# Performance work log

Hardware: AMD Instinct MI355X
Metric: run time of the kernel (lower is better)

The kernel has to match this reference:

```python
import jax, jax.numpy as jnp
import numpy as np

N = 100000
E = 1600000
D_IN = 64
D_OUT = 64
EPS = 1e-5  # PyG LayerNorm eps


def setup_inputs() -> dict:
    key = jax.random.key(0)
    k1, k2, k3, k4 = jax.random.split(key, 4)
    x = jax.random.normal(k1, (N, D_IN), dtype=jnp.float32)
    edge_index = jax.random.randint(k2, (2, E), 0, N, dtype=jnp.int32)
    edge_weight = jax.random.uniform(k3, (E,), dtype=jnp.float32)
    # GCNConv params: Linear(D_IN, D_OUT, bias=True) -> weight [D_OUT, D_IN]
    W = jax.random.normal(k4, (D_OUT, D_IN), dtype=jnp.float32) * (1.0 / np.sqrt(D_IN))
    b = jnp.zeros((D_OUT,), dtype=jnp.float32)
    # LayerNorm affine params (per-feature)
    gamma = jnp.ones((D_OUT,), dtype=jnp.float32)
    beta = jnp.zeros((D_OUT,), dtype=jnp.float32)
    return {"x": x, "edge_index": edge_index, "edge_weight": edge_weight,
            "W": W, "b": b, "gamma": gamma, "beta": beta}


def reference(x, edge_index, edge_weight, W, b, gamma, beta):
    # --- GCNConv with symmetric normalization and self-loops ---
    n = x.shape[0]
    loop = jnp.arange(n, dtype=edge_index.dtype)
    src = jnp.concatenate([edge_index[0], loop])          # [E+N]
    dst = jnp.concatenate([edge_index[1], loop])          # [E+N]
    w = jnp.concatenate([edge_weight, jnp.ones((n,), x.dtype)])
    deg = jax.ops.segment_sum(w, dst, num_segments=n)     # weighted in-degree
    dis = jnp.where(deg > 0, jax.lax.rsqrt(deg), 0.0)     # deg^{-1/2}
    norm = dis[src] * w * dis[dst]                        # [E+N]
    xw = x @ W.T                                          # [N, D_OUT]
    msgs = xw[src] * norm[:, None]                        # gather + scale
    out = jax.ops.segment_sum(msgs, dst, num_segments=n) + b
    # --- PyG LayerNorm mode='graph' (single graph): mean/var over all entries ---
    mu = out.mean()
    var = jnp.mean((out - mu) ** 2)
    out = (out - mu) * jax.lax.rsqrt(var + EPS) * gamma + beta
    # --- activation (ReLU), norm_first=False -> act(norm(x)) ---
    return jax.nn.relu(out)
```

## Files before the change

kernel.cpp:

```cpp
#include <hip/hip_runtime.h>
#include <hip/hip_fp16.h>
#include <math.h>

#define D 64
#define LN_EPS 1e-5f
#define SCAN_CH 1024
#define WFIX 262144.0f
#define CNT_SH 25
#define WSUM_MASK ((1u << CNT_SH) - 1)
#define WQ_BITS 15
#define WQ_SCALE 32768.0f
#define NB 1024
#define BSH 7
#define GP 256


__global__ __launch_bounds__(256) void k_hist1(const int* __restrict__ ei, int E,
                                               int* __restrict__ hist) {
    __shared__ int h[NB];
    for (int i = threadIdx.x; i < NB; i += 256) h[i] = 0;
    __syncthreads();
    int chunk = (E + GP - 1) / GP;
    int s0 = blockIdx.x * chunk;
    int s1 = min(E, s0 + chunk);
    for (int e = s0 + threadIdx.x; e < s1; e += 256)
        atomicAdd(&h[((unsigned int)ei[E + e]) >> BSH], 1);
    __syncthreads();
    for (int i = threadIdx.x; i < NB; i += 256)
        hist[i * GP + blockIdx.x] = h[i];
}

__global__ __launch_bounds__(256) void k_scanb(int* __restrict__ hist,
                                               int* __restrict__ total) {
    int lane = threadIdx.x & 63, wv = threadIdx.x >> 6;
    int bucket = blockIdx.x * 4 + wv;
    int4 c = *(int4*)&hist[bucket * GP + lane * 4];
    int lsum = c.x + c.y + c.z + c.w;
    int sum = lsum;
#pragma unroll
    for (int off2 = 1; off2 < 64; off2 <<= 1) {
        int t = __shfl_up(sum, off2);
        if (lane >= off2) sum += t;
    }
    int base = sum - lsum;
    int4 o;
    o.x = base; o.y = base + c.x; o.z = o.y + c.y; o.w = o.z + c.z;
    *(int4*)&hist[bucket * GP + lane * 4] = o;
    if (lane == 63) total[bucket] = sum;
}

__global__ __launch_bounds__(SCAN_CH) void k_scan_base(int* __restrict__ psum, int nblk) {
    __shared__ int s[SCAN_CH];
    int tid = threadIdx.x;
    s[tid] = (tid < nblk) ? psum[tid] : 0;
    __syncthreads();
    int own = s[tid];
    for (int off = 1; off < SCAN_CH; off <<= 1) {
        int t = (tid >= off) ? s[tid - off] : 0;
        __syncthreads();
        s[tid] += t;
        __syncthreads();
    }
    if (tid < nblk) psum[tid] = s[tid] - own;
}

__global__ __launch_bounds__(256) void k_part(const int* __restrict__ ei,
                                              const float* __restrict__ w,
                                              const int* __restrict__ hist,
                                              const int* __restrict__ total,
                                              unsigned long long* __restrict__ part,
                                              int E) {
    __shared__ int cur[NB];
    for (int i = threadIdx.x; i < NB; i += 256)
        cur[i] = total[i] + hist[i * GP + blockIdx.x];
    __syncthreads();
    int chunk = (E + GP - 1) / GP;
    int s0 = blockIdx.x * chunk;
    int s1 = min(E, s0 + chunk);
    for (int e = s0 + threadIdx.x; e < s1; e += 256) {
        unsigned int dst = (unsigned int)ei[E + e];
        unsigned int src = (unsigned int)ei[e];
        float wf = w[e];
        int pos = atomicAdd(&cur[dst >> BSH], 1);
        unsigned int wq = __float2uint_rn(wf * WQ_SCALE);
        if (wq > 32767u) wq = 32767u;
        unsigned int wfix = __float2uint_rn(wf * WFIX);
        unsigned int lo = (src << WQ_BITS) | wq;
        unsigned int hi = (dst & ((1u << BSH) - 1)) | (wfix << BSH);
        part[pos] = ((unsigned long long)hi << 32) | lo;
    }
}

__global__ __launch_bounds__(256) void k_emit(const unsigned long long* __restrict__ part,
                                              const int* __restrict__ total,
                                              unsigned int* __restrict__ packed,
                                              int* __restrict__ nstart,
                                              unsigned int* __restrict__ csr,
                                              int N, int E) {
    __shared__ unsigned int cw[1 << BSH];
    __shared__ int cursor[1 << BSH];
    __shared__ int wtot[2];
    int b = blockIdx.x;
    int beg = total[b];
    int end = (b == NB - 1) ? E : total[b + 1];
    int tid = threadIdx.x;
    if (tid < (1 << BSH)) cw[tid] = 0;
    __syncthreads();
    for (int i = beg + tid; i < end; i += 256) {
        unsigned int hi = (unsigned int)(part[i] >> 32);
        atomicAdd(&cw[hi & 127u], (1u << CNT_SH) | (hi >> BSH));
    }
    __syncthreads();
    int lane = tid & 63, wv = tid >> 6;
    if (tid < 128) {
        unsigned int p = cw[tid];
        int cnt = (int)(p >> CNT_SH);
        int sum = cnt;
#pragma unroll
        for (int off2 = 1; off2 < 64; off2 <<= 1) {
            int t = __shfl_up(sum, off2);
            if (lane >= off2) sum += t;
        }
        if (lane == 63) wtot[wv] = sum;
        cursor[tid] = sum - cnt;
        int node = (b << BSH) + tid;
        if (node < N) packed[node] = p;
    }
    __syncthreads();
    if (tid < 128) {
        int st = cursor[tid] + beg + ((wv == 1) ? wtot[0] : 0);
        cursor[tid] = st;
        int node = (b << BSH) + tid;
        if (node < N) nstart[node] = st;
    }
    __syncthreads();
    for (int i = beg + tid; i < end; i += 256) {
        unsigned long long r = part[i];
        unsigned int hi = (unsigned int)(r >> 32);
        int pos = atomicAdd(&cursor[hi & 127u], 1);
        csr[pos] = (unsigned int)r;
    }
}

__global__ __launch_bounds__(256, 4) void k_gemm(const float* __restrict__ x,
                                                 const float* __restrict__ W,
                                                 const unsigned int* __restrict__ packed,
                                                 __half* __restrict__ y, int N) {
    __shared__ float Ws[D * 68];
    __shared__ float xs[64 * 68];
    int tid = threadIdx.x;
    int rowBase = blockIdx.x * 64;
#pragma unroll
    for (int i = 0; i < 16; ++i) {
        int idx = i * 256 + tid;
        int a = idx >> 6, kk = idx & 63;
        Ws[a * 68 + kk] = W[idx];
        int row = rowBase + a;
        xs[a * 68 + kk] = (row < N) ? x[idx + rowBase * D] : 0.0f;
    }
    __syncthreads();
    int l = tid & 63, wv = tid >> 6;
    int g = l >> 4;
    int c1 = l & 15;
    int r0 = wv * 16 + g * 4;
    float acc[4][4];
#pragma unroll
    for (int a = 0; a < 4; ++a)
#pragma unroll
        for (int bj = 0; bj < 4; ++bj) acc[a][bj] = 0.0f;
#pragma unroll 2
    for (int kc = 0; kc < 16; ++kc) {
        int k0 = kc * 4;
        float4 xr[4], wr[4];
#pragma unroll
        for (int jr = 0; jr < 4; ++jr)
            xr[jr] = *(const float4*)&xs[(r0 + jr) * 68 + k0];
#pragma unroll
        for (int jc = 0; jc < 4; ++jc)
            wr[jc] = *(const float4*)&Ws[(c1 + 16 * jc) * 68 + k0];
#pragma unroll
        for (int jr = 0; jr < 4; ++jr)
#pragma unroll
            for (int jc = 0; jc < 4; ++jc)
                acc[jr][jc] += xr[jr].x * wr[jc].x + xr[jr].y * wr[jc].y +
                               xr[jr].z * wr[jc].z + xr[jr].w * wr[jc].w;
    }
#pragma unroll
    for (int jr = 0; jr < 4; ++jr) {
        int row = rowBase + r0 + jr;
        if (row < N) {
            float dr = rsqrtf(1.0f +
                (float)(packed[row] & WSUM_MASK) * (1.0f / WFIX));
#pragma unroll
            for (int jc = 0; jc < 4; ++jc)
                y[row * D + c1 + 16 * jc] = __float2half_rn(acc[jr][jc] * dr);
        }
    }
}

__global__ __launch_bounds__(256) void k_gather(const unsigned int* __restrict__ packed,
                                                const int* __restrict__ nstart,
                                                const unsigned int* __restrict__ csr,
                                                const __half* __restrict__ y,
                                                const float* __restrict__ b,
                                                float* __restrict__ out,
                                                float* __restrict__ partial, int N) {
    int wid = (blockIdx.x * 256 + threadIdx.x) >> 6;
    int lane = threadIdx.x & 63;
    float s = 0.0f, ss = 0.0f;
    if (wid < N) {
        int n = wid;
        unsigned int p = packed[n];
        int m = (int)(p >> CNT_SH);
        int start = nstart[n];
        float dis_n = rsqrtf(1.0f + (float)(p & WSUM_MASK) * (1.0f / WFIX));
        float acc = __half2float(y[(size_t)n * D + lane]);
        const float wsc = 1.0f / WQ_SCALE;
        for (int base0 = start; base0 < start + m; base0 += 64) {
            int mm = start + m - base0; if (mm > 64) mm = 64;
            unsigned int pe = (lane < mm) ? csr[base0 + lane] : 0u;
            int j = 0;
            for (; j + 3 < mm; j += 4) {
                unsigned int p0 = __shfl(pe, j);
                unsigned int p1 = __shfl(pe, j + 1);
                unsigned int p2 = __shfl(pe, j + 2);
                unsigned int p3 = __shfl(pe, j + 3);
                float a0 = __half2float(y[(size_t)(p0 >> WQ_BITS) * D + lane]);
                float a1 = __half2float(y[(size_t)(p1 >> WQ_BITS) * D + lane]);
                float a2 = __half2float(y[(size_t)(p2 >> WQ_BITS) * D + lane]);
                float a3 = __half2float(y[(size_t)(p3 >> WQ_BITS) * D + lane]);
                acc += (float)(p0 & 32767u) * wsc * a0;
                acc += (float)(p1 & 32767u) * wsc * a1;
                acc += (float)(p2 & 32767u) * wsc * a2;
                acc += (float)(p3 & 32767u) * wsc * a3;
            }
            for (; j < mm; ++j) {
                unsigned int p0 = __shfl(pe, j);
                acc += (float)(p0 & 32767u) * wsc *
                       __half2float(y[(size_t)(p0 >> WQ_BITS) * D + lane]);
            }
        }
        float o = dis_n * acc + b[lane];
        out[(size_t)n * D + lane] = o;
        s = o;
        ss = o * o;
    }
#pragma unroll
    for (int off = 32; off; off >>= 1) {
        s += __shfl_down(s, off);
        ss += __shfl_down(ss, off);
    }
    __shared__ float ls[4], lss[4];
    int wv = threadIdx.x >> 6;
    if (lane == 0) { ls[wv] = s; lss[wv] = ss; }
    __syncthreads();
    if (threadIdx.x == 0) {
        partial[2 * blockIdx.x]     = ls[0] + ls[1] + ls[2] + ls[3];
        partial[2 * blockIdx.x + 1] = lss[0] + lss[1] + lss[2] + lss[3];
    }
}

__global__ __launch_bounds__(SCAN_CH) void k_redux(const float* __restrict__ partial,
                                                   int nb, double* __restrict__ scal) {
    double s = 0.0, ss = 0.0;
    for (int i = threadIdx.x; i < nb; i += SCAN_CH) {
        s += (double)partial[2 * i];
        ss += (double)partial[2 * i + 1];
    }
#pragma unroll
    for (int off = 32; off; off >>= 1) {
        s += __shfl_down(s, off);
        ss += __shfl_down(ss, off);
    }
    __shared__ double ls[SCAN_CH / 64], lss[SCAN_CH / 64];
    int lane = threadIdx.x & 63, wv = threadIdx.x >> 6;
    if (lane == 0) { ls[wv] = s; lss[wv] = ss; }
    __syncthreads();
    if (threadIdx.x == 0) {
        double S = 0.0, SS = 0.0;
        for (int k = 0; k < SCAN_CH / 64; ++k) { S += ls[k]; SS += lss[k]; }
        scal[0] = S;
        scal[1] = SS;
    }
}

__global__ __launch_bounds__(256) void k_ln(float* __restrict__ out,
                                            const float* __restrict__ gamma,
                                            const float* __restrict__ beta,
                                            const double* __restrict__ scal, int N) {
    int nchunks = N * (D / 4);
    int i = blockIdx.x * blockDim.x + threadIdx.x;
    if (i >= nchunks) return;
    double M = (double)N * (double)D;
    double mu = scal[0] / M;
    double var = scal[1] / M - mu * mu;
    float muf = (float)mu;
    float isd = (float)(1.0 / sqrt(var + (double)LN_EPS));
    int c4 = (i & 15) * 4;
    float4 v = ((float4*)out)[i];
    v.x = fmaxf((v.x - muf) * isd * gamma[c4 + 0] + beta[c4 + 0], 0.0f);
    v.y = fmaxf((v.y - muf) * isd * gamma[c4 + 1] + beta[c4 + 1], 0.0f);
    v.z = fmaxf((v.z - muf) * isd * gamma[c4 + 2] + beta[c4 + 2], 0.0f);
    v.w = fmaxf((v.w - muf) * isd * gamma[c4 + 3] + beta[c4 + 3], 0.0f);
    ((float4*)out)[i] = v;
}

__global__ __launch_bounds__(256) void k_build(const int* __restrict__ ei,
                                               const float* __restrict__ w,
                                               unsigned int* __restrict__ packed,
                                               int E) {
    int e = blockIdx.x * blockDim.x + threadIdx.x;
    if (e < E) {
        unsigned int v = (1u << CNT_SH) | __float2uint_rn(w[e] * WFIX);
        atomicAdd(&packed[ei[E + e]], v);
    }
}

__global__ __launch_bounds__(256) void k_scatter(const int* __restrict__ ei,
                                                 const float* __restrict__ w,
                                                 const __half* __restrict__ y,
                                                 float* __restrict__ out, int E) {
    int t = blockIdx.x * blockDim.x + threadIdx.x;
    int e = t >> 6;
    int lane = t & 63;
    if (e >= E) return;
    float v = w[e] * __half2float(y[(size_t)ei[e] * D + lane]);
    unsafeAtomicAdd(&out[(size_t)ei[E + e] * D + lane], v);
}

__global__ __launch_bounds__(256) void k_seed(const __half* __restrict__ y,
                                              float* __restrict__ out, int total) {
    int i = blockIdx.x * blockDim.x + threadIdx.x;
    if (i < total) out[i] = __half2float(y[i]);
}

__global__ __launch_bounds__(256) void k_finalize(float* __restrict__ out,
                                                  const unsigned int* __restrict__ packed,
                                                  const float* __restrict__ b,
                                                  double* __restrict__ scal, int N) {
    int nchunks = N * (D / 4);
    float s = 0.0f, ss = 0.0f;
    float4* o4 = (float4*)out;
    for (int i = blockIdx.x * blockDim.x + threadIdx.x; i < nchunks;
         i += gridDim.x * blockDim.x) {
        int row = i >> 4;
        int c4 = (i & 15) * 4;
        float4 v = o4[i];
        float dr = rsqrtf(1.0f + (float)(packed[row] & WSUM_MASK) * (1.0f / WFIX));
        v.x = dr * v.x + b[c4 + 0];
        v.y = dr * v.y + b[c4 + 1];
        v.z = dr * v.z + b[c4 + 2];
        v.w = dr * v.w + b[c4 + 3];
        o4[i] = v;
        s += v.x + v.y + v.z + v.w;
        ss += v.x * v.x + v.y * v.y + v.z * v.z + v.w * v.w;
    }
#pragma unroll
    for (int off = 32; off; off >>= 1) {
        s += __shfl_down(s, off);
        ss += __shfl_down(ss, off);
    }
    __shared__ float ls[4], lss[4];
    int lane = threadIdx.x & 63, wv = threadIdx.x >> 6;
    if (lane == 0) { ls[wv] = s; lss[wv] = ss; }
    __syncthreads();
    if (threadIdx.x == 0) {
        atomicAdd(&scal[0], (double)(ls[0] + ls[1] + ls[2] + ls[3]));
        atomicAdd(&scal[1], (double)(lss[0] + lss[1] + lss[2] + lss[3]));
    }
}

extern "C" void kernel_launch(void* const* d_in, const int* in_sizes, int n_in,
                              void* d_out, int out_size, void* d_ws, size_t ws_size,
                              hipStream_t stream) {
    const float* x     = (const float*)d_in[0];
    const int*   ei    = (const int*)d_in[1];
    const float* ew    = (const float*)d_in[2];
    const float* W     = (const float*)d_in[3];
    const float* b     = (const float*)d_in[4];
    const float* gamma = (const float*)d_in[5];
    const float* beta  = (const float*)d_in[6];
    float* out = (float*)d_out;

    int N = in_sizes[0] / D;
    int E = in_sizes[2];
    int gb = (N + 3) / 4;

    char* ws = (char*)d_ws;
    size_t off = 0;
    unsigned int* packed = (unsigned int*)(ws + off); off += (size_t)N * 4;
    int* nstart  = (int*)(ws + off);    off += (size_t)N * 4;
    int* hist    = (int*)(ws + off);    off += (size_t)NB * GP * 4;
    int* total   = (int*)(ws + off);    off += (size_t)NB * 4;
    double* scal = (double*)(ws + off); off += 16;
    float* partial = (float*)(ws + off); off += (size_t)gb * 8;
    off = (off + 255) & ~(size_t)255;
    size_t partBytes = (size_t)E * 8;
    size_t yBytes = (size_t)N * D * 2;
    unsigned long long* part = (unsigned long long*)(ws + off);
    __half* y = (__half*)(ws + off);
    off += (partBytes > yBytes) ? partBytes : yBytes;
    off = (off + 255) & ~(size_t)255;
    unsigned int* csr = (unsigned int*)(ws + off); off += (size_t)E * 4;

    int nbu = (N + (1 << BSH) - 1) >> BSH;
    bool csr_path = (ws_size >= off) && (N <= (1 << 17)) && (nbu <= NB) &&
                    ((size_t)E <= (size_t)N * 24);

    if (csr_path) {
        k_hist1<<<GP, 256, 0, stream>>>(ei, E, hist);
        k_scanb<<<NB / 4, 256, 0, stream>>>(hist, total);
        k_scan_base<<<1, SCAN_CH, 0, stream>>>(total, NB);
        k_part<<<GP, 256, 0, stream>>>(ei, ew, hist, total, part, E);
        k_emit<<<nbu, 256, 0, stream>>>(part, total, packed, nstart, csr, N, E);
        k_gemm<<<(N + 63) / 64, 256, 0, stream>>>(x, W, packed, y, N);
        k_gather<<<gb, 256, 0, stream>>>(packed, nstart, csr, y, b, out, partial, N);
        k_redux<<<1, SCAN_CH, 0, stream>>>(partial, gb, scal);
        k_ln<<<(N * (D / 4) + 255) / 256, 256, 0, stream>>>(out, gamma, beta, scal, N);
    } else {
        hipMemsetAsync(packed, 0, (size_t)N * 4, stream);
        hipMemsetAsync(scal, 0, 16, stream);
        k_build<<<(E + 255) / 256, 256, 0, stream>>>(ei, ew, packed, E);
        k_gemm<<<(N + 63) / 64, 256, 0, stream>>>(x, W, packed, y, N);
        k_seed<<<(N * D + 255) / 256, 256, 0, stream>>>(y, out, N * D);
        k_scatter<<<(E + 3) / 4, 256, 0, stream>>>(ei, ew, y, out, E);
        k_finalize<<<2048, 256, 0, stream>>>(out, packed, b, scal, N);
        k_ln<<<(N * (D / 4) + 255) / 256, 256, 0, stream>>>(out, gamma, beta, scal, N);
    }
}
```

Before: 241.6 us.

## Fuse scan and reduction kernels; grid-stride gather with scalar CSR loads

The single-block base scan is folded into the partition kernel: each block recomputes the 1024-entry bucket prefix itself and block 0 writes it out for the emit stage. The separate stats reduction kernel is removed, and every LayerNorm block now re-reduces the 2048 gather partials in double before normalising. The gather becomes a grid-stride loop over a fixed 2048-block grid, reading CSR entries as wave-uniform scalar loads instead of a lane load plus shuffles. Two launches are removed, at the cost of redundant per-block prefix and reduction work.

```diff
diff --git a/kernel.cpp b/kernel.cpp
--- a/kernel.cpp
+++ b/kernel.cpp
@@ -13,6 +13,7 @@
 #define NB 1024
 #define BSH 7
 #define GP 256
+#define GB2 2048
 
 
 __global__ __launch_bounds__(256) void k_hist1(const int* __restrict__ ei, int E,
@@ -49,39 +50,52 @@
     if (lane == 63) total[bucket] = sum;
 }
 
-__global__ __launch_bounds__(SCAN_CH) void k_scan_base(int* __restrict__ psum, int nblk) {
-    __shared__ int s[SCAN_CH];
+__global__ __launch_bounds__(256) void k_part2(const int* __restrict__ ei,
+                                               const float* __restrict__ w,
+                                               const int* __restrict__ hist,
+                                               const int* __restrict__ total,
+                                               int* __restrict__ total2,
+                                               unsigned long long* __restrict__ part,
+                                               int E) {
+    __shared__ int shB[NB];
+    __shared__ int shA[NB];
+    __shared__ int wt4[4];
     int tid = threadIdx.x;
-    s[tid] = (tid < nblk) ? psum[tid] : 0;
-    __syncthreads();
-    int own = s[tid];
-    for (int off = 1; off < SCAN_CH; off <<= 1) {
-        int t = (tid >= off) ? s[tid - off] : 0;
+    int lane = tid & 63, wv = tid >> 6;
+    {
+        int4 c4v = *(const int4*)&total[tid * 4];
+        int lsum = c4v.x + c4v.y + c4v.z + c4v.w;
+        int sum = lsum;
+#pragma unroll
+        for (int o2 = 1; o2 < 64; o2 <<= 1) {
+            int t = __shfl_up(sum, o2);
+            if (lane >= o2) sum += t;
+        }
+        if (lane == 63) wt4[wv] = sum;
         __syncthreads();
-        s[tid] += t;
-        __syncthreads();
-    }
-    if (tid < nblk) psum[tid] = s[tid] - own;
-}
-
-__global__ __launch_bounds__(256) void k_part(const int* __restrict__ ei,
-                                              const float* __restrict__ w,
-                                              const int* __restrict__ hist,
-                                              const int* __restrict__ total,
-                                              unsigned long long* __restrict__ part,
-                                              int E) {
-    __shared__ int cur[NB];
-    for (int i = threadIdx.x; i < NB; i += 256)
-        cur[i] = total[i] + hist[i * GP + blockIdx.x];
+        int woff = 0;
+#pragma unroll
+        for (int k = 0; k < 4; ++k) if (k < wv) woff += wt4[k];
+        int base = woff + sum - lsum;
+        shB[tid * 4 + 0] = base;
+        shB[tid * 4 + 1] = base + c4v.x;
+        shB[tid * 4 + 2] = base + c4v.x + c4v.y;
+        shB[tid * 4 + 3] = base + c4v.x + c4v.y + c4v.z;
+    }
+    __syncthreads();
+    if (blockIdx.x == 0)
+        *(int4*)&total2[tid * 4] = *(const int4*)&shB[tid * 4];
+    for (int i = tid; i < NB; i += 256)
+        shA[i] = shB[i] + hist[i * GP + blockIdx.x];
     __syncthreads();
     int chunk = (E + GP - 1) / GP;
     int s0 = blockIdx.x * chunk;
     int s1 = min(E, s0 + chunk);
-    for (int e = s0 + threadIdx.x; e < s1; e += 256) {
+    for (int e = s0 + tid; e < s1; e += 256) {
         unsigned int dst = (unsigned int)ei[E + e];
         unsigned int src = (unsigned int)ei[e];
         float wf = w[e];
-        int pos = atomicAdd(&cur[dst >> BSH], 1);
+        int pos = atomicAdd(&shA[dst >> BSH], 1);
         unsigned int wq = __float2uint_rn(wf * WQ_SCALE);
         if (wq > 32767u) wq = 32767u;
         unsigned int wfix = __float2uint_rn(wf * WFIX);
@@ -92,7 +106,7 @@
 }
 
 __global__ __launch_bounds__(256) void k_emit(const unsigned long long* __restrict__ part,
-                                              const int* __restrict__ total,
+                                              const int* __restrict__ total2,
                                               unsigned int* __restrict__ packed,
                                               int* __restrict__ nstart,
                                               unsigned int* __restrict__ csr,
@@ -101,8 +115,8 @@
     __shared__ int cursor[1 << BSH];
     __shared__ int wtot[2];
     int b = blockIdx.x;
-    int beg = total[b];
-    int end = (b == NB - 1) ? E : total[b + 1];
+    int beg = total2[b];
+    int end = (b == NB - 1) ? E : total2[b + 1];
     int tid = threadIdx.x;
     if (tid < (1 << BSH)) cw[tid] = 0;
     __syncthreads();
@@ -117,9 +131,9 @@
         int cnt = (int)(p >> CNT_SH);
         int sum = cnt;
 #pragma unroll
-        for (int off2 = 1; off2 < 64; off2 <<= 1) {
-            int t = __shfl_up(sum, off2);
-            if (lane >= off2) sum += t;
+        for (int o2 = 1; o2 < 64; o2 <<= 1) {
+            int t = __shfl_up(sum, o2);
+            if (lane >= o2) sum += t;
         }
         if (lane == 63) wtot[wv] = sum;
         cursor[tid] = sum - cnt;
@@ -198,52 +212,50 @@
     }
 }
 
-__global__ __launch_bounds__(256) void k_gather(const unsigned int* __restrict__ packed,
-                                                const int* __restrict__ nstart,
-                                                const unsigned int* __restrict__ csr,
-                                                const __half* __restrict__ y,
-                                                const float* __restrict__ b,
-                                                float* __restrict__ out,
-                                                float* __restrict__ partial, int N) {
-    int wid = (blockIdx.x * 256 + threadIdx.x) >> 6;
-    int lane = threadIdx.x & 63;
+__global__ __launch_bounds__(256) void k_gather2(const unsigned int* __restrict__ packed,
+                                                 const int* __restrict__ nstart,
+                                                 const unsigned int* __restrict__ csr,
+                                                 const __half* __restrict__ y,
+                                                 const float* __restrict__ bias,
+                                                 float* __restrict__ out,
+                                                 float* __restrict__ partial, int N) {
+    int tid = threadIdx.x;
+    int lane = tid & 63, wv = tid >> 6;
+    int gwave = blockIdx.x * 4 + wv;
+    int nwaves = gridDim.x * 4;
     float s = 0.0f, ss = 0.0f;
-    if (wid < N) {
-        int n = wid;
+    const float wsc = 1.0f / WQ_SCALE;
+    float bl = bias[lane];
+    for (int n = gwave; n < N; n += nwaves) {
         unsigned int p = packed[n];
-        int m = (int)(p >> CNT_SH);
-        int start = nstart[n];
+        int m = __builtin_amdgcn_readfirstlane((int)(p >> CNT_SH));
+        int su = __builtin_amdgcn_readfirstlane(nstart[n]);
         float dis_n = rsqrtf(1.0f + (float)(p & WSUM_MASK) * (1.0f / WFIX));
         float acc = __half2float(y[(size_t)n * D + lane]);
-        const float wsc = 1.0f / WQ_SCALE;
-        for (int base0 = start; base0 < start + m; base0 += 64) {
-            int mm = start + m - base0; if (mm > 64) mm = 64;
-            unsigned int pe = (lane < mm) ? csr[base0 + lane] : 0u;
-            int j = 0;
-            for (; j + 3 < mm; j += 4) {
-                unsigned int p0 = __shfl(pe, j);
-                unsigned int p1 = __shfl(pe, j + 1);
-                unsigned int p2 = __shfl(pe, j + 2);
-                unsigned int p3 = __shfl(pe, j + 3);
-                float a0 = __half2float(y[(size_t)(p0 >> WQ_BITS) * D + lane]);
-                float a1 = __half2float(y[(size_t)(p1 >> WQ_BITS) * D + lane]);
-                float a2 = __half2float(y[(size_t)(p2 >> WQ_BITS) * D + lane]);
-                float a3 = __half2float(y[(size_t)(p3 >> WQ_BITS) * D + lane]);
-                acc += (float)(p0 & 32767u) * wsc * a0;
-                acc += (float)(p1 & 32767u) * wsc * a1;
-                acc += (float)(p2 & 32767u) * wsc * a2;
-                acc += (float)(p3 & 32767u) * wsc * a3;
-            }
-            for (; j < mm; ++j) {
-                unsigned int p0 = __shfl(pe, j);
-                acc += (float)(p0 & 32767u) * wsc *
-                       __half2float(y[(size_t)(p0 >> WQ_BITS) * D + lane]);
-            }
+        int j = 0;
+        for (; j + 3 < m; j += 4) {
+            unsigned int p0 = csr[su + j];
+            unsigned int p1 = csr[su + j + 1];
+            unsigned int p2 = csr[su + j + 2];
+            unsigned int p3 = csr[su + j + 3];
+            float a0 = __half2float(y[(size_t)(p0 >> WQ_BITS) * D + lane]);
+            float a1 = __half2float(y[(size_t)(p1 >> WQ_BITS) * D + lane]);
+            float a2 = __half2float(y[(size_t)(p2 >> WQ_BITS) * D + lane]);
+            float a3 = __half2float(y[(size_t)(p3 >> WQ_BITS) * D + lane]);
+            acc += (float)(p0 & 32767u) * wsc * a0;
+            acc += (float)(p1 & 32767u) * wsc * a1;
+            acc += (float)(p2 & 32767u) * wsc * a2;
+            acc += (float)(p3 & 32767u) * wsc * a3;
         }
-        float o = dis_n * acc + b[lane];
+        for (; j < m; ++j) {
+            unsigned int p0 = csr[su + j];
+            acc += (float)(p0 & 32767u) * wsc *
+                   __half2float(y[(size_t)(p0 >> WQ_BITS) * D + lane]);
+        }
+        float o = dis_n * acc + bl;
         out[(size_t)n * D + lane] = o;
-        s = o;
-        ss = o * o;
+        s += o;
+        ss += o * o;
     }
 #pragma unroll
     for (int off = 32; off; off >>= 1) {
@@ -251,51 +263,49 @@
         ss += __shfl_down(ss, off);
     }
     __shared__ float ls[4], lss[4];
-    int wv = threadIdx.x >> 6;
     if (lane == 0) { ls[wv] = s; lss[wv] = ss; }
     __syncthreads();
-    if (threadIdx.x == 0) {
+    if (tid == 0) {
         partial[2 * blockIdx.x]     = ls[0] + ls[1] + ls[2] + ls[3];
         partial[2 * blockIdx.x + 1] = lss[0] + lss[1] + lss[2] + lss[3];
     }
 }
 
-__global__ __launch_bounds__(SCAN_CH) void k_redux(const float* __restrict__ partial,
-                                                   int nb, double* __restrict__ scal) {
-    double s = 0.0, ss = 0.0;
-    for (int i = threadIdx.x; i < nb; i += SCAN_CH) {
-        s += (double)partial[2 * i];
-        ss += (double)partial[2 * i + 1];
+__global__ __launch_bounds__(256) void k_ln2(float* __restrict__ out,
+                                             const float* __restrict__ gamma,
+                                             const float* __restrict__ beta,
+                                             const float* __restrict__ partial,
+                                             int N) {
+    __shared__ double dls[4], dlss[4];
+    __shared__ float mu_s, isd_s;
+    int tid = threadIdx.x;
+    int lane = tid & 63, wv = tid >> 6;
+    double ds = 0.0, dss = 0.0;
+    for (int i = tid; i < GB2; i += 256) {
+        ds += (double)partial[2 * i];
+        dss += (double)partial[2 * i + 1];
     }
 #pragma unroll
     for (int off = 32; off; off >>= 1) {
-        s += __shfl_down(s, off);
-        ss += __shfl_down(ss, off);
-    }
-    __shared__ double ls[SCAN_CH / 64], lss[SCAN_CH / 64];
-    int lane = threadIdx.x & 63, wv = threadIdx.x >> 6;
-    if (lane == 0) { ls[wv] = s; lss[wv] = ss; }
-    __syncthreads();
-    if (threadIdx.x == 0) {
-        double S = 0.0, SS = 0.0;
-        for (int k = 0; k < SCAN_CH / 64; ++k) { S += ls[k]; SS += lss[k]; }
-        scal[0] = S;
-        scal[1] = SS;
-    }
-}
-
-__global__ __launch_bounds__(256) void k_ln(float* __restrict__ out,
-                                            const float* __restrict__ gamma,
-                                            const float* __restrict__ beta,
-                                            const double* __restrict__ scal, int N) {
+        ds += __shfl_down(ds, off);
+        dss += __shfl_down(dss, off);
+    }
+    if (lane == 0) { dls[wv] = ds; dlss[wv] = dss; }
+    __syncthreads();
+    if (tid == 0) {
+        double S = dls[0] + dls[1] + dls[2] + dls[3];
+        double SS = dlss[0] + dlss[1] + dlss[2] + dlss[3];
+        double M = (double)N * (double)D;
+        double mu = S / M;
+        double var = SS / M - mu * mu;
+        mu_s = (float)mu;
+        isd_s = (float)(1.0 / sqrt(var + (double)LN_EPS));
+    }
+    __syncthreads();
+    float muf = mu_s, isd = isd_s;
     int nchunks = N * (D / 4);
-    int i = blockIdx.x * blockDim.x + threadIdx.x;
+    int i = blockIdx.x * 256 + tid;
     if (i >= nchunks) return;
-    double M = (double)N * (double)D;
-    double mu = scal[0] / M;
-    double var = scal[1] / M - mu * mu;
-    float muf = (float)mu;
-    float isd = (float)(1.0 / sqrt(var + (double)LN_EPS));
     int c4 = (i & 15) * 4;
     float4 v = ((float4*)out)[i];
     v.x = fmaxf((v.x - muf) * isd * gamma[c4 + 0] + beta[c4 + 0], 0.0f);
@@ -370,6 +380,27 @@
     }
 }
 
+__global__ __launch_bounds__(256) void k_ln(float* __restrict__ out,
+                                            const float* __restrict__ gamma,
+                                            const float* __restrict__ beta,
+                                            const double* __restrict__ scal, int N) {
+    int nchunks = N * (D / 4);
+    int i = blockIdx.x * blockDim.x + threadIdx.x;
+    if (i >= nchunks) return;
+    double M = (double)N * (double)D;
+    double mu = scal[0] / M;
+    double var = scal[1] / M - mu * mu;
+    float muf = (float)mu;
+    float isd = (float)(1.0 / sqrt(var + (double)LN_EPS));
+    int c4 = (i & 15) * 4;
+    float4 v = ((float4*)out)[i];
+    v.x = fmaxf((v.x - muf) * isd * gamma[c4 + 0] + beta[c4 + 0], 0.0f);
+    v.y = fmaxf((v.y - muf) * isd * gamma[c4 + 1] + beta[c4 + 1], 0.0f);
+    v.z = fmaxf((v.z - muf) * isd * gamma[c4 + 2] + beta[c4 + 2], 0.0f);
+    v.w = fmaxf((v.w - muf) * isd * gamma[c4 + 3] + beta[c4 + 3], 0.0f);
+    ((float4*)out)[i] = v;
+}
+
 extern "C" void kernel_launch(void* const* d_in, const int* in_sizes, int n_in,
                               void* d_out, int out_size, void* d_ws, size_t ws_size,
                               hipStream_t stream) {
@@ -384,16 +415,17 @@
 
     int N = in_sizes[0] / D;
     int E = in_sizes[2];
-    int gb = (N + 3) / 4;
 
     char* ws = (char*)d_ws;
     size_t off = 0;
     unsigned int* packed = (unsigned int*)(ws + off); off += (size_t)N * 4;
     int* nstart  = (int*)(ws + off);    off += (size_t)N * 4;
+    off = (off + 255) & ~(size_t)255;
     int* hist    = (int*)(ws + off);    off += (size_t)NB * GP * 4;
     int* total   = (int*)(ws + off);    off += (size_t)NB * 4;
+    int* total2  = (int*)(ws + off);    off += (size_t)NB * 4;
     double* scal = (double*)(ws + off); off += 16;
-    float* partial = (float*)(ws + off); off += (size_t)gb * 8;
+    float* partial = (float*)(ws + off); off += (size_t)GB2 * 8;
     off = (off + 255) & ~(size_t)255;
     size_t partBytes = (size_t)E * 8;
     size_t yBytes = (size_t)N * D * 2;
@@ -404,19 +436,20 @@
     unsigned int* csr = (unsigned int*)(ws + off); off += (size_t)E * 4;
 
     int nbu = (N + (1 << BSH) - 1) >> BSH;
-    bool csr_path = (ws_size >= off) && (N <= (1 << 17)) && (nbu <= NB) &&
+    bool csr_path = (ws_size >= off) && (nbu <= NB) &&
+                    (N < (1 << (32 - WQ_BITS))) &&
                     ((size_t)E <= (size_t)N * 24);
 
     if (csr_path) {
         k_hist1<<<GP, 256, 0, stream>>>(ei, E, hist);
         k_scanb<<<NB / 4, 256, 0, stream>>>(hist, total);
-        k_scan_base<<<1, SCAN_CH, 0, stream>>>(total, NB);
-        k_part<<<GP, 256, 0, stream>>>(ei, ew, hist, total, part, E);
-        k_emit<<<nbu, 256, 0, stream>>>(part, total, packed, nstart, csr, N, E);
+        k_part2<<<GP, 256, 0, stream>>>(ei, ew, hist, total, total2, part, E);
+        k_emit<<<nbu, 256, 0, stream>>>(part, total2, packed, nstart, csr, N, E);
         k_gemm<<<(N + 63) / 64, 256, 0, stream>>>(x, W, packed, y, N);
-        k_gather<<<gb, 256, 0, stream>>>(packed, nstart, csr, y, b, out, partial, N);
-        k_redux<<<1, SCAN_CH, 0, stream>>>(partial, gb, scal);
-        k_ln<<<(N * (D / 4) + 255) / 256, 256, 0, stream>>>(out, gamma, beta, scal, N);
+        k_gather2<<<GB2, 256, 0, stream>>>(packed, nstart, csr, y, b, out,
+                                           partial, N);
+        k_ln2<<<(N * (D / 4) + 255) / 256, 256, 0, stream>>>(out, gamma, beta,
+                                                             partial, N);
     } else {
         hipMemsetAsync(packed, 0, (size_t)N * 4, stream);
         hipMemsetAsync(scal, 0, 16, stream);
```

Measured after the change: 221.4 us. -8.3%, faster.
